# Kernel optimization log

Measured on AMD Instinct MI355X. Metric: run time of the kernel, lower is better.

Reference implementation:

```python
import jax, jax.numpy as jnp
import numpy as np

B, N, T, D, E, M = 8, 512, 64, 128, 32, 3


def _norm(v):
    return v / jnp.clip(jnp.linalg.norm(v, axis=-1, keepdims=True), 1e-12)


def setup_inputs() -> dict:
    key = jax.random.key(0)
    ks = jax.random.split(key, 14)
    s = 0.05
    x = jax.random.normal(ks[0], (B, N, T, 1), jnp.float32)
    # set_prior: binarized adjacency + self loops, row-normalized
    a = (jax.random.uniform(ks[1], (N, N)) > 0.95).astype(jnp.float32) + jnp.eye(N, dtype=jnp.float32)
    prior = a / jnp.clip(a.sum(1, keepdims=True), 1e-8)
    # orthogonal queries, as in torch __init__ (QR of zero-padded randn)
    rng = np.random.default_rng(0)
    qs = []
    for _ in range(M):
        pad = np.zeros((D, D), np.float32)
        pad[:E] = rng.standard_normal((E, D)).astype(np.float32) * 0.1
        q, _ = np.linalg.qr(pad)
        qs.append(q[:E])
    return {
        "x": x,
        "prior": prior,
        "proj_W": jax.random.normal(ks[2], (D, 1), jnp.float32) * s,
        "proj_b": jnp.zeros((D,), jnp.float32),
        "W_ih": jax.random.normal(ks[3], (3 * D, D), jnp.float32) * s,
        "W_hh": jax.random.normal(ks[4], (3 * D, D), jnp.float32) * s,
        "b_ih": jnp.zeros((3 * D,), jnp.float32),
        "b_hh": jnp.zeros((3 * D,), jnp.float32),
        "space_W": jax.random.normal(ks[5], (M, D, D), jnp.float32) * s,
        "space_b": jnp.zeros((M, D), jnp.float32),
        "router_W": jax.random.normal(ks[6], (M, 2 * D), jnp.float32) * s,
        "router_b": jnp.zeros((M,), jnp.float32),
        "out_W": jax.random.normal(ks[7], (1, D), jnp.float32) * s,
        "out_b": jnp.zeros((1,), jnp.float32),
        "prior_logit": jnp.array(1.0, jnp.float32),
        "queries": jnp.asarray(np.stack(qs)),  # [M, E, D]
    }


def reference(x, prior, proj_W, proj_b, W_ih, W_hh, b_ih, b_hh,
              space_W, space_b, router_W, router_b, out_W, out_b,
              prior_logit, queries):
    b, n, t, _ = x.shape
    d = proj_b.shape[0]
    m, e, _ = queries.shape
    # proj(x.permute(0,2,1,3)).reshape(B*N, T, D)  (faithful reshape of [B,T,N,D])
    hp = jnp.transpose(x, (0, 2, 1, 3)) @ proj_W.T + proj_b  # [B,T,N,D]
    seq = hp.reshape(b * n, t, d)
    xs = jnp.swapaxes(seq, 0, 1)  # [T, BN, D]

    def gru_step(h, xt):
        gi = xt @ W_ih.T + b_ih
        gh = h @ W_hh.T + b_hh
        ir, iz, i_n = jnp.split(gi, 3, axis=-1)
        hr, hz, h_n = jnp.split(gh, 3, axis=-1)
        r = jax.nn.sigmoid(ir + hr)
        z = jax.nn.sigmoid(iz + hz)
        ng = jnp.tanh(i_n + r * h_n)
        return (1.0 - z) * ng + z * h, None

    h, _ = jax.lax.scan(gru_step, jnp.zeros((b * n, d), x.dtype), xs)
    h = h.reshape(b, n, d)

    stats = jnp.concatenate([h.mean(1), jnp.std(h, axis=1, ddof=1)], axis=-1)  # torch std is unbiased
    probs = jax.nn.softmax(stats @ router_W.T + router_b, axis=-1)  # [B,M]

    z_prior = jnp.einsum('ij,bjd->bid', prior, h)

    hs = _norm(jnp.einsum('bnd,mkd->bmnk', h, space_W) + space_b[None, :, None, :])  # [B,M,N,D]
    q = _norm(queries)  # [M,E,D]
    scores = jnp.einsum('bmnd,med->bmen', hs, q)  # [B,M,E,N] (topk over N axis)
    k = min(n, max(4, int(n * 0.05)))
    vals, idx = jax.lax.top_k(scores, k)  # [B,M,E,k]
    w = jax.nn.softmax(vals / 0.7, axis=-1)
    H = jnp.zeros((b, m, e, n), h.dtype).at[
        jnp.arange(b)[:, None, None, None],
        jnp.arange(m)[None, :, None, None],
        jnp.arange(e)[None, None, :, None],
        idx,
    ].set(w)  # [B,M,E,N], transposed layout of torch's [B,N,E]

    Hmix = jnp.einsum('bmen,bm->ben', H, probs)  # [B,E,N] == torch Hmix^T
    edge = jnp.einsum('ben,bnd->bed', Hmix, h)   # Hmix^T @ h
    z_learn = jnp.einsum('ben,bed->bnd', Hmix, edge)  # Hmix @ edge

    alpha = jax.nn.sigmoid(prior_logit)
    out = (alpha * z_prior + (1.0 - alpha) * z_learn) @ out_W.T + out_b  # [B,N,1]
    return out.squeeze(-1), probs
```

## Files before the change

kernel.cpp:

```cpp
#include <hip/hip_runtime.h>
#include <math.h>

#define OFF_U      0
#define OFF_C      384
#define OFF_QWHI   768
#define OFF_QWLO   6912
#define OFF_H      13056
#define OFF_PROBS  537344
#define OFF_HV     537376
#define OFF_SCORES 541472
#define OFF_HMIX   934688
#define OFF_WHI    1066016
#define OFF_SHI    1115168
#define OFF_SLO    1139744
#define OFF_STATS  1164320
#define OFF_EV     1229856
#define OFF_QB     1230112

#define L2E_F 1.44269504088896340736f

typedef short bf16x8 __attribute__((ext_vector_type(8)));
typedef float f32x4 __attribute__((ext_vector_type(4)));

union U8 { unsigned short s[8]; bf16x8 v; uint4 u4; };

__device__ __forceinline__ unsigned short bf16_rtn(float f) {
  unsigned int u = __float_as_uint(f);
  return (unsigned short)((u + 0x7FFFu + ((u >> 16) & 1u)) >> 16);
}
__device__ __forceinline__ float bf16_f(unsigned short h) {
  return __uint_as_float(((unsigned int)h) << 16);
}

__global__ __launch_bounds__(256) void prep_kernel(const float* __restrict__ Wih,
                                                   const float* __restrict__ projW,
                                                   const float* __restrict__ projb,
                                                   const float* __restrict__ bih,
                                                   const float* __restrict__ queries,
                                                   const float* __restrict__ Whh,
                                                   const float* __restrict__ spaceW,
                                                   const float* __restrict__ spaceb,
                                                   float* __restrict__ ws) {
  const int bid = blockIdx.x, tid = threadIdx.x;
  const int wave = tid >> 6, lane = tid & 63;
  if (bid < 96) {
    int r = bid * 4 + wave;
    float w0 = Wih[r * 128 + lane], w1 = Wih[r * 128 + 64 + lane];
    float u = w0 * projW[lane] + w1 * projW[64 + lane];
    float c = w0 * projb[lane] + w1 * projb[64 + lane];
    for (int off = 32; off; off >>= 1) {
      u += __shfl_xor(u, off);
      c += __shfl_xor(c, off);
    }
    if (lane == 0) {
      ws[OFF_U + r] = u;
      ws[OFF_C + r] = c + bih[r];
    }
  } else if (bid < 112) {
    unsigned short* WHI = (unsigned short*)(ws + OFF_WHI);
    int base = (bid - 96) * 3072;
    for (int i = tid; i < 3072; i += 256) {
      int idx = base + i;
      float sc = (idx < 32768) ? L2E_F : (2.f * L2E_F);
      WHI[idx] = bf16_rtn(Whh[idx] * sc);
    }
  } else if (bid < 128) {
    unsigned short* SHI = (unsigned short*)(ws + OFF_SHI);
    unsigned short* SLO = (unsigned short*)(ws + OFF_SLO);
    int base = (bid - 112) * 3072;
    for (int i = tid; i < 3072; i += 256) {
      float w = spaceW[base + i];
      unsigned short hi = bf16_rtn(w);
      SHI[base + i] = hi;
      SLO[base + i] = bf16_rtn(w - bf16_f(hi));
    }
  } else if (bid < 224) {
    int qi = bid - 128;
    int m = qi >> 5, e = qi & 31;
    __shared__ float invS, qdS;
    const float* qrow = queries + (m * 32 + e) * 128;
    if (wave == 0) {
      float v0 = qrow[lane], v1 = qrow[64 + lane];
      float ss = v0 * v0 + v1 * v1;
      for (int off = 32; off; off >>= 1) ss += __shfl_xor(ss, off);
      if (lane == 0) invS = 1.f / fmaxf(sqrtf(ss), 1e-12f);
    } else if (wave == 1) {
      float v = qrow[lane] * spaceb[m * 128 + lane] +
                qrow[64 + lane] * spaceb[m * 128 + 64 + lane];
      for (int off = 32; off; off >>= 1) v += __shfl_xor(v, off);
      if (lane == 0) qdS = v;
    }
    __syncthreads();
    if (tid < 128) {
      int din = tid;
      float acc = 0.f;
      for (int dout = 0; dout < 128; ++dout)
        acc += qrow[dout] * spaceW[m * 16384 + dout * 128 + din];
      acc *= invS;
      unsigned short hi = bf16_rtn(acc);
      ((unsigned short*)(ws + OFF_QWHI))[(m * 32 + e) * 128 + din] = hi;
      ((unsigned short*)(ws + OFF_QWLO))[(m * 32 + e) * 128 + din] =
          bf16_rtn(acc - bf16_f(hi));
    }
    if (tid == 255) ws[OFF_QB + m * 32 + e] = qdS * invS;
  } else {
    ws[OFF_EV + tid] = 0.f;
    for (int i = tid; i < 2048; i += 256) ws[OFF_STATS + i] = 0.f;
  }
}

#define GRU_STEP(RB, WB, XSV)                                                       \
  do {                                                                              \
    f32x4 acc0 = c0i, acc1 = c1i, acc2 = c2i;                                       \
    _Pragma("unroll") for (int c = 0; c < 4; ++c) {                                 \
      bf16x8 Bf = *(const bf16x8*)&hB[RB][rdOff + c * 32];                          \
      acc0 = __builtin_amdgcn_mfma_f32_16x16x32_bf16(Bf, Ah[0][c], acc0, 0, 0, 0);  \
      acc1 = __builtin_amdgcn_mfma_f32_16x16x32_bf16(Bf, Ah[1][c], acc1, 0, 0, 0);  \
      acc2 = __builtin_amdgcn_mfma_f32_16x16x32_bf16(Bf, Ah[2][c], acc2, 0, 0, 0);  \
    }                                                                               \
    const float xsv = (XSV);                                                        \
    float hv[4];                                                                    \
    _Pragma("unroll") for (int r = 0; r < 4; ++r) {                                 \
      float gr = fmaf(xsv, ur[r], acc0[r]);                                         \
      float gz = fmaf(xsv, uz[r], acc1[r]);                                         \
      float gn = fmaf(xsv, un[r], cnv[r]);                                          \
      float rr = __builtin_amdgcn_rcpf(1.f + __builtin_amdgcn_exp2f(-gr));          \
      float Ez = __builtin_amdgcn_exp2f(gz);                                        \
      float a = fmaf(rr, acc2[r], gn);                                              \
      float Ea = __builtin_amdgcn_exp2f(a);                                         \
      float u = Ea + 1.f;                                                           \
      float v = Ez + 1.f;                                                           \
      float num = fmaf(1.f - hreg[r], u, -2.f);                                     \
      float hvv = fmaf(num, __builtin_amdgcn_rcpf(u * v), hreg[r]);                 \
      hv[r] = hvv;                                                                  \
      hreg[r] = hvv;                                                                \
    }                                                                               \
    unsigned int pk0, pk1;                                                          \
    asm("v_cvt_pk_bf16_f32 %0, %1, %2" : "=v"(pk0) : "v"(hv[0]), "v"(hv[1]));       \
    asm("v_cvt_pk_bf16_f32 %0, %1, %2" : "=v"(pk1) : "v"(hv[2]), "v"(hv[3]));       \
    *(uint2*)&hB[WB][wrOff] = make_uint2(pk0, pk1);                                 \
    __syncthreads();                                                                \
  } while (0)

__global__ __launch_bounds__(512, 2) void gru_kernel(const float* __restrict__ x,
                                                     const float* __restrict__ bhh,
                                                     const float* __restrict__ outW,
                                                     float* __restrict__ ws) {
  __shared__ __align__(16) unsigned short hB[2][16 * 136];
  __shared__ __align__(16) float xsAll[16 * 68];
  __shared__ float hFin[16 * 132];

  const int tid = threadIdx.x, wave = tid >> 6, lane = tid & 63;
  const int q = lane >> 4, s15 = lane & 15;
  const int d0 = wave * 16 + q * 4;
  const unsigned short* WHI = (const unsigned short*)(ws + OFF_WHI);

  {
    float4 z4 = make_float4(0.f, 0.f, 0.f, 0.f);
    float4* hm4 = (float4*)(ws + OFF_HMIX);
    if (tid < 128) hm4[blockIdx.x * 128 + tid] = z4;
  }

  bf16x8 Ah[3][4];
#pragma unroll
  for (int t = 0; t < 3; ++t) {
    int row = (wave + 8 * t) * 16 + s15;
#pragma unroll
    for (int c = 0; c < 4; ++c)
      Ah[t][c] = *(const bf16x8*)&WHI[row * 128 + c * 32 + q * 8];
  }

  float ur[4], uz[4], un[4], cnv[4];
  f32x4 c0i, c1i, c2i;
#pragma unroll
  for (int r = 0; r < 4; ++r) {
    int d = d0 + r;
    ur[r] = ws[OFF_U + d] * L2E_F;
    uz[r] = ws[OFF_U + 128 + d] * L2E_F;
    un[r] = ws[OFF_U + 256 + d] * (2.f * L2E_F);
    c0i[r] = (ws[OFF_C + d] + bhh[d]) * L2E_F;
    c1i[r] = (ws[OFF_C + 128 + d] + bhh[128 + d]) * L2E_F;
    cnv[r] = ws[OFF_C + 256 + d] * (2.f * L2E_F);
    c2i[r] = bhh[256 + d] * (2.f * L2E_F);
  }

  const int seq0 = blockIdx.x * 16;
  for (int i = tid; i < 1024; i += 512) {
    int s = i >> 6, tt = i & 63;
    int r = (seq0 + s) * 64 + tt;
    xsAll[s * 68 + tt] = x[((r >> 15) * 512 + (r & 511)) * 64 + ((r >> 9) & 63)];
  }
  for (int i = tid; i < 2176; i += 512) hB[0][i] = 0;
  __syncthreads();

  float hreg[4] = {0.f, 0.f, 0.f, 0.f};
  const int rdOff = s15 * 136 + q * 8;
  const int wrOff = s15 * 136 + d0;
  const int xsOff = s15 * 68;

#pragma unroll 1
  for (int t4 = 0; t4 < 16; ++t4) {
    const float4 xs4 = *(const float4*)&xsAll[xsOff + t4 * 4];
    GRU_STEP(0, 1, xs4.x);
    GRU_STEP(1, 0, xs4.y);
    GRU_STEP(0, 1, xs4.z);
    GRU_STEP(1, 0, xs4.w);
  }

#pragma unroll
  for (int r = 0; r < 4; ++r) hFin[s15 * 132 + d0 + r] = hreg[r];
  __syncthreads();
  float* h_out = ws + OFF_H;
#pragma unroll
  for (int p = 0; p < 4; ++p) {
    int item = tid + p * 512;
    int s = item >> 7, dd = item & 127;
    h_out[(seq0 + s) * 128 + dd] = hFin[s * 132 + dd];
  }
  for (int s = wave * 2; s < wave * 2 + 2; ++s) {
    float a = hFin[s * 132 + lane] * outW[lane] + hFin[s * 132 + 64 + lane] * outW[64 + lane];
    for (int off = 32; off; off >>= 1) a += __shfl_xor(a, off);
    if (lane == 0) ws[OFF_HV + seq0 + s] = a;
  }
  if (tid < 128) {
    float s = 0.f, q2 = 0.f;
#pragma unroll
    for (int sI = 0; sI < 16; ++sI) {
      float v = hFin[sI * 132 + tid];
      s += v; q2 += v * v;
    }
    int b = blockIdx.x >> 5;
    atomicAdd(&ws[OFF_STATS + b * 256 + tid], s);
    atomicAdd(&ws[OFF_STATS + b * 256 + 128 + tid], q2);
  }
}

__global__ __launch_bounds__(256) void scores_kernel(const float* __restrict__ spaceb,
                                                     const float* __restrict__ routerW,
                                                     const float* __restrict__ routerb,
                                                     float* __restrict__ ws,
                                                     float* __restrict__ d_out) {
  const int bid = blockIdx.x;
  const int chunk = bid & 15, m = (bid >> 4) % 3, b = bid / 48;
  const int n0 = chunk * 32;
  const int tid = threadIdx.x, wave = tid >> 6, lane = tid & 63;
  const int q = lane >> 4, s15 = lane & 15;

  __shared__ __align__(16) unsigned short sHi[16 * 33 * 8];
  __shared__ __align__(16) unsigned short sLo[16 * 33 * 8];
  __shared__ float hsL[32 * 132];
  __shared__ float biasL[128];
  __shared__ float invnL[32];
  __shared__ float qbL[32];

  const float* hG = ws + OFF_H;
  const unsigned short* SHI = (const unsigned short*)(ws + OFF_SHI);
  const unsigned short* SLO = (const unsigned short*)(ws + OFF_SLO);
  const unsigned short* QWHI = (const unsigned short*)(ws + OFF_QWHI);
  const unsigned short* QWLO = (const unsigned short*)(ws + OFF_QWLO);

  if (tid < 128) biasL[tid] = spaceb[m * 128 + tid];
  else if (tid < 160) qbL[tid - 128] = ws[OFF_QB + m * 32 + (tid - 128)];
  {
    int nn = tid >> 3, kc = tid & 7;
    const float* row = &hG[(b * 512 + n0 + nn) * 128 + kc * 16];
    U8 ph0, pl0, ph1, pl1;
#pragma unroll
    for (int j = 0; j < 8; ++j) {
      float v = row[j];
      unsigned short hi = bf16_rtn(v);
      ph0.s[j] = hi; pl0.s[j] = bf16_rtn(v - bf16_f(hi));
    }
#pragma unroll
    for (int j = 0; j < 8; ++j) {
      float v = row[8 + j];
      unsigned short hi = bf16_rtn(v);
      ph1.s[j] = hi; pl1.s[j] = bf16_rtn(v - bf16_f(hi));
    }
    int g0 = kc * 2;
    *(uint4*)&sHi[(g0 * 33 + nn) * 8] = ph0.u4;
    *(uint4*)&sLo[(g0 * 33 + nn) * 8] = pl0.u4;
    *(uint4*)&sHi[((g0 + 1) * 33 + nn) * 8] = ph1.u4;
    *(uint4*)&sLo[((g0 + 1) * 33 + nn) * 8] = pl1.u4;
  }
  __syncthreads();

  const int nt = wave >> 1;
  const int half = wave & 1;
  const int dt0 = half * 4;
  f32x4 acc[4] = {{0.f,0.f,0.f,0.f},{0.f,0.f,0.f,0.f},{0.f,0.f,0.f,0.f},{0.f,0.f,0.f,0.f}};
  f32x4 accS = {0.f, 0.f, 0.f, 0.f};
#pragma unroll
  for (int c = 0; c < 4; ++c) {
    bf16x8 Ahi = *(const bf16x8*)&sHi[((c * 4 + q) * 33 + nt * 16 + s15) * 8];
    bf16x8 Alo = *(const bf16x8*)&sLo[((c * 4 + q) * 33 + nt * 16 + s15) * 8];
#pragma unroll
    for (int i = 0; i < 4; ++i) {
      int row = m * 16384 + ((dt0 + i) * 16 + s15) * 128 + c * 32 + q * 8;
      bf16x8 Bhi = *(const bf16x8*)&SHI[row];
      bf16x8 Blo = *(const bf16x8*)&SLO[row];
      acc[i] = __builtin_amdgcn_mfma_f32_16x16x32_bf16(Ahi, Bhi, acc[i], 0, 0, 0);
      acc[i] = __builtin_amdgcn_mfma_f32_16x16x32_bf16(Alo, Bhi, acc[i], 0, 0, 0);
      acc[i] = __builtin_amdgcn_mfma_f32_16x16x32_bf16(Ahi, Blo, acc[i], 0, 0, 0);
    }
    {
      int row = (m * 32 + half * 16 + s15) * 128 + c * 32 + q * 8;
      bf16x8 Qhi = *(const bf16x8*)&QWHI[row];
      bf16x8 Qlo = *(const bf16x8*)&QWLO[row];
      accS = __builtin_amdgcn_mfma_f32_16x16x32_bf16(Ahi, Qhi, accS, 0, 0, 0);
      accS = __builtin_amdgcn_mfma_f32_16x16x32_bf16(Alo, Qhi, accS, 0, 0, 0);
      accS = __builtin_amdgcn_mfma_f32_16x16x32_bf16(Ahi, Qlo, accS, 0, 0, 0);
    }
  }
#pragma unroll
  for (int i = 0; i < 4; ++i) {
    int dcol = (dt0 + i) * 16 + s15;
    float bb = biasL[dcol];
#pragma unroll
    for (int r = 0; r < 4; ++r)
      hsL[(nt * 16 + q * 4 + r) * 132 + dcol] = acc[i][r] + bb;
  }
  __syncthreads();

  {
    int n = tid >> 3, kc = tid & 7;
    float ss = 0.f;
#pragma unroll
    for (int d4 = 0; d4 < 4; ++d4) {
      float4 v = *(const float4*)&hsL[n * 132 + kc * 16 + d4 * 4];
      ss += v.x * v.x + v.y * v.y + v.z * v.z + v.w * v.w;
    }
    ss += __shfl_xor(ss, 1); ss += __shfl_xor(ss, 2); ss += __shfl_xor(ss, 4);
    if (kc == 0) invnL[n] = 1.f / fmaxf(sqrtf(ss), 1e-12f);
  }
  __syncthreads();

  {
    int e = half * 16 + s15;
    float qb = qbL[e];
    int nb = nt * 16 + q * 4;
    float4 o;
    o.x = (accS[0] + qb) * invnL[nb + 0];
    o.y = (accS[1] + qb) * invnL[nb + 1];
    o.z = (accS[2] + qb) * invnL[nb + 2];
    o.w = (accS[3] + qb) * invnL[nb + 3];
    *(float4*)&ws[OFF_SCORES + ((b * 3 + m) * 32 + e) * 512 + n0 + nb] = o;
  }

  if ((bid % 48) == 0) {
    __syncthreads();
    float* st = hsL;
    float* lgS = hsL + 256;
    if (tid < 128) {
      float s = ws[OFF_STATS + b * 256 + tid];
      float q2 = ws[OFF_STATS + b * 256 + 128 + tid];
      float mean = s * (1.f / 512.f);
      float var = (q2 - 512.f * mean * mean) * (1.f / 511.f);
      st[tid] = mean;
      st[128 + tid] = sqrtf(fmaxf(var, 0.f));
    }
    __syncthreads();
    if (tid < 192) {
      int w = tid >> 6, ln = tid & 63;
      float acc2 = 0.f;
#pragma unroll
      for (int j = 0; j < 4; ++j)
        acc2 += st[ln * 4 + j] * routerW[w * 256 + ln * 4 + j];
      for (int off = 32; off; off >>= 1) acc2 += __shfl_xor(acc2, off);
      if (ln == 0) lgS[w] = acc2 + routerb[w];
    }
    __syncthreads();
    if (tid == 0) {
      float mx = fmaxf(lgS[0], fmaxf(lgS[1], lgS[2]));
      float e0 = expf(lgS[0] - mx), e1 = expf(lgS[1] - mx), e2 = expf(lgS[2] - mx);
      float inv = 1.f / (e0 + e1 + e2);
      ws[OFF_PROBS + b * 3 + 0] = e0 * inv;
      ws[OFF_PROBS + b * 3 + 1] = e1 * inv;
      ws[OFF_PROBS + b * 3 + 2] = e2 * inv;
      d_out[4096 + b * 3 + 0] = e0 * inv;
      d_out[4096 + b * 3 + 1] = e1 * inv;
      d_out[4096 + b * 3 + 2] = e2 * inv;
    }
  }
}

__global__ __launch_bounds__(256) void topk_kernel(float* __restrict__ ws) {
  const int row0 = blockIdx.x * 4;
  const int b = row0 / 96;
  const int tid = threadIdx.x, wave = tid >> 6, lane = tid & 63;
  __shared__ float hvL[512];
  hvL[tid] = ws[OFF_HV + b * 512 + tid];
  hvL[256 + tid] = ws[OFF_HV + b * 512 + 256 + tid];
  __syncthreads();

  int row = row0 + wave;
  int m = (row / 32) % 3, e = row & 31;
  const float* sc = ws + OFF_SCORES + row * 512;
  float prob = ws[OFF_PROBS + b * 3 + m];

  float v[8];
#pragma unroll
  for (int j = 0; j < 8; ++j) v[j] = sc[j * 64 + lane];

  float selv = 0.f; int seli = 0; float maxv = 0.f;
  for (int it = 0; it < 25; ++it) {
    float bv = v[0]; int bj = 0;
#pragma unroll
    for (int j = 1; j < 8; ++j)
      if (v[j] > bv) { bv = v[j]; bj = j; }
    int bidx = bj * 64 + lane;
    for (int off = 32; off; off >>= 1) {
      float ov = __shfl_xor(bv, off);
      int oi = __shfl_xor(bidx, off);
      if (ov > bv || (ov == bv && oi < bidx)) { bv = ov; bidx = oi; }
    }
    if (lane == (bidx & 63)) v[bidx >> 6] = -INFINITY;
    if (it == 0) maxv = bv;
    if (lane == it) { selv = bv; seli = bidx; }
  }
  float ex = (lane < 25) ? __expf((selv - maxv) * (1.f / 0.7f)) : 0.f;
  float den = ex;
  for (int off = 32; off; off >>= 1) den += __shfl_xor(den, off);
  float w = prob * ex / den;
  if (lane < 25)
    atomicAdd(&ws[OFF_HMIX + (b * 32 + e) * 512 + seli], w);
  float evc = (lane < 25) ? w * hvL[seli] : 0.f;
  for (int off = 32; off; off >>= 1) evc += __shfl_xor(evc, off);
  if (lane == 0) atomicAdd(&ws[OFF_EV + b * 32 + e], evc);
}

__global__ __launch_bounds__(512) void final_kernel(const float* __restrict__ prior,
                                                    const float* __restrict__ outb,
                                                    const float* __restrict__ plog,
                                                    float* __restrict__ ws,
                                                    float* __restrict__ d_out) {
  const int bid = blockIdx.x;
  const int b = bid >> 4, ch = bid & 15;
  const int tid = threadIdx.x, wave = tid >> 6, lane = tid & 63;
  __shared__ float hvL[512], evL[32];
  hvL[tid] = ws[OFF_HV + b * 512 + tid];
  if (tid < 32) evL[tid] = ws[OFF_EV + b * 32 + tid];
  __syncthreads();
  float alpha = 1.f / (1.f + expf(-plog[0]));
  float ob = outb[0];
#pragma unroll
  for (int i = 0; i < 4; ++i) {
    int n = ch * 32 + wave * 4 + i;
    const float* pr = prior + n * 512;
    float s1 = 0.f;
#pragma unroll
    for (int j = 0; j < 8; ++j) s1 += pr[j * 64 + lane] * hvL[j * 64 + lane];
    float s2 = 0.f;
    if (lane < 32) s2 = ws[OFF_HMIX + (b * 32 + lane) * 512 + n] * evL[lane];
    float a = alpha * s1 + (1.f - alpha) * s2;
    for (int off = 32; off; off >>= 1) a += __shfl_xor(a, off);
    if (lane == 0) d_out[b * 512 + n] = a + ob;
  }
}

extern "C" void kernel_launch(void* const* d_in, const int* in_sizes, int n_in,
                              void* d_out, int out_size, void* d_ws, size_t ws_size,
                              hipStream_t stream) {
  const float* x       = (const float*)d_in[0];
  const float* prior   = (const float*)d_in[1];
  const float* projW   = (const float*)d_in[2];
  const float* projb   = (const float*)d_in[3];
  const float* Wih     = (const float*)d_in[4];
  const float* Whh     = (const float*)d_in[5];
  const float* bih     = (const float*)d_in[6];
  const float* bhh     = (const float*)d_in[7];
  const float* spaceW  = (const float*)d_in[8];
  const float* spaceb  = (const float*)d_in[9];
  const float* routerW = (const float*)d_in[10];
  const float* routerb = (const float*)d_in[11];
  const float* outW    = (const float*)d_in[12];
  const float* outb    = (const float*)d_in[13];
  const float* plog    = (const float*)d_in[14];
  const float* queries = (const float*)d_in[15];
  float* ws  = (float*)d_ws;
  float* out = (float*)d_out;

  prep_kernel<<<225, 256, 0, stream>>>(Wih, projW, projb, bih, queries, Whh,
                                       spaceW, spaceb, ws);
  gru_kernel<<<256, 512, 0, stream>>>(x, bhh, outW, ws);
  scores_kernel<<<384, 256, 0, stream>>>(spaceb, routerW, routerb, ws, out);
  topk_kernel<<<192, 256, 0, stream>>>(ws);
  final_kernel<<<128, 512, 0, stream>>>(prior, outb, plog, ws, out);
}
```

Measured before the change: 162.2 us.

## Fuse scores, topk and final kernels into one persistent kernel with grid barriers

Merges the scores, top-k and final kernels into a single launch of 384 blocks, separated by global atomic-counter barriers with spin-waits. Blocks that finish early exit at each phase (192 run top-k, 128 run the final stage, each now covering 8 rows per wave). The aim is to drop two kernel launch gaps. In exchange it relies on all 384 blocks being co-resident to avoid deadlock, and the spin-waits add polling cost.

```diff
diff --git a/kernel.cpp b/kernel.cpp
--- a/kernel.cpp
+++ b/kernel.cpp
@@ -16,6 +16,7 @@
 #define OFF_STATS  1164320
 #define OFF_EV     1229856
 #define OFF_QB     1230112
+#define OFF_SYNC   1230208
 
 #define L2E_F 1.44269504088896340736f
 
@@ -106,6 +107,7 @@
   } else {
     ws[OFF_EV + tid] = 0.f;
     for (int i = tid; i < 2048; i += 256) ws[OFF_STATS + i] = 0.f;
+    if (tid < 2) ((unsigned int*)(ws + OFF_SYNC))[tid] = 0u;
   }
 }
 
@@ -235,14 +237,15 @@
   }
 }
 
-__global__ __launch_bounds__(256) void scores_kernel(const float* __restrict__ spaceb,
-                                                     const float* __restrict__ routerW,
-                                                     const float* __restrict__ routerb,
-                                                     float* __restrict__ ws,
-                                                     float* __restrict__ d_out) {
+__global__ __launch_bounds__(256) void fused_kernel(const float* __restrict__ spaceb,
+                                                    const float* __restrict__ routerW,
+                                                    const float* __restrict__ routerb,
+                                                    const float* __restrict__ prior,
+                                                    const float* __restrict__ outb,
+                                                    const float* __restrict__ plog,
+                                                    float* __restrict__ ws,
+                                                    float* __restrict__ d_out) {
   const int bid = blockIdx.x;
-  const int chunk = bid & 15, m = (bid >> 4) % 3, b = bid / 48;
-  const int n0 = chunk * 32;
   const int tid = threadIdx.x, wave = tid >> 6, lane = tid & 63;
   const int q = lane >> 4, s15 = lane & 15;
 
@@ -252,209 +255,237 @@
   __shared__ float biasL[128];
   __shared__ float invnL[32];
   __shared__ float qbL[32];
-
-  const float* hG = ws + OFF_H;
-  const unsigned short* SHI = (const unsigned short*)(ws + OFF_SHI);
-  const unsigned short* SLO = (const unsigned short*)(ws + OFF_SLO);
-  const unsigned short* QWHI = (const unsigned short*)(ws + OFF_QWHI);
-  const unsigned short* QWLO = (const unsigned short*)(ws + OFF_QWLO);
-
-  if (tid < 128) biasL[tid] = spaceb[m * 128 + tid];
-  else if (tid < 160) qbL[tid - 128] = ws[OFF_QB + m * 32 + (tid - 128)];
+  __shared__ float hvT[512];
+  __shared__ float hvF[512];
+  __shared__ float evL[32];
+
+  unsigned int* cnt = (unsigned int*)(ws + OFF_SYNC);
+
   {
-    int nn = tid >> 3, kc = tid & 7;
-    const float* row = &hG[(b * 512 + n0 + nn) * 128 + kc * 16];
-    U8 ph0, pl0, ph1, pl1;
-#pragma unroll
-    for (int j = 0; j < 8; ++j) {
-      float v = row[j];
-      unsigned short hi = bf16_rtn(v);
-      ph0.s[j] = hi; pl0.s[j] = bf16_rtn(v - bf16_f(hi));
-    }
-#pragma unroll
-    for (int j = 0; j < 8; ++j) {
-      float v = row[8 + j];
-      unsigned short hi = bf16_rtn(v);
-      ph1.s[j] = hi; pl1.s[j] = bf16_rtn(v - bf16_f(hi));
-    }
-    int g0 = kc * 2;
-    *(uint4*)&sHi[(g0 * 33 + nn) * 8] = ph0.u4;
-    *(uint4*)&sLo[(g0 * 33 + nn) * 8] = pl0.u4;
-    *(uint4*)&sHi[((g0 + 1) * 33 + nn) * 8] = ph1.u4;
-    *(uint4*)&sLo[((g0 + 1) * 33 + nn) * 8] = pl1.u4;
-  }
+    const int chunk = bid & 15, m = (bid >> 4) % 3, b = bid / 48;
+    const int n0 = chunk * 32;
+
+    const float* hG = ws + OFF_H;
+    const unsigned short* SHI = (const unsigned short*)(ws + OFF_SHI);
+    const unsigned short* SLO = (const unsigned short*)(ws + OFF_SLO);
+    const unsigned short* QWHI = (const unsigned short*)(ws + OFF_QWHI);
+    const unsigned short* QWLO = (const unsigned short*)(ws + OFF_QWLO);
+
+    if (tid < 128) biasL[tid] = spaceb[m * 128 + tid];
+    else if (tid < 160) qbL[tid - 128] = ws[OFF_QB + m * 32 + (tid - 128)];
+    {
+      int nn = tid >> 3, kc = tid & 7;
+      const float* row = &hG[(b * 512 + n0 + nn) * 128 + kc * 16];
+      U8 ph0, pl0, ph1, pl1;
+#pragma unroll
+      for (int j = 0; j < 8; ++j) {
+        float v = row[j];
+        unsigned short hi = bf16_rtn(v);
+        ph0.s[j] = hi; pl0.s[j] = bf16_rtn(v - bf16_f(hi));
+      }
+#pragma unroll
+      for (int j = 0; j < 8; ++j) {
+        float v = row[8 + j];
+        unsigned short hi = bf16_rtn(v);
+        ph1.s[j] = hi; pl1.s[j] = bf16_rtn(v - bf16_f(hi));
+      }
+      int g0 = kc * 2;
+      *(uint4*)&sHi[(g0 * 33 + nn) * 8] = ph0.u4;
+      *(uint4*)&sLo[(g0 * 33 + nn) * 8] = pl0.u4;
+      *(uint4*)&sHi[((g0 + 1) * 33 + nn) * 8] = ph1.u4;
+      *(uint4*)&sLo[((g0 + 1) * 33 + nn) * 8] = pl1.u4;
+    }
+    __syncthreads();
+
+    const int nt = wave >> 1;
+    const int half = wave & 1;
+    const int dt0 = half * 4;
+    f32x4 acc[4] = {{0.f,0.f,0.f,0.f},{0.f,0.f,0.f,0.f},{0.f,0.f,0.f,0.f},{0.f,0.f,0.f,0.f}};
+    f32x4 accS = {0.f, 0.f, 0.f, 0.f};
+#pragma unroll
+    for (int c = 0; c < 4; ++c) {
+      bf16x8 Ahi = *(const bf16x8*)&sHi[((c * 4 + q) * 33 + nt * 16 + s15) * 8];
+      bf16x8 Alo = *(const bf16x8*)&sLo[((c * 4 + q) * 33 + nt * 16 + s15) * 8];
+#pragma unroll
+      for (int i = 0; i < 4; ++i) {
+        int row = m * 16384 + ((dt0 + i) * 16 + s15) * 128 + c * 32 + q * 8;
+        bf16x8 Bhi = *(const bf16x8*)&SHI[row];
+        bf16x8 Blo = *(const bf16x8*)&SLO[row];
+        acc[i] = __builtin_amdgcn_mfma_f32_16x16x32_bf16(Ahi, Bhi, acc[i], 0, 0, 0);
+        acc[i] = __builtin_amdgcn_mfma_f32_16x16x32_bf16(Alo, Bhi, acc[i], 0, 0, 0);
+        acc[i] = __builtin_amdgcn_mfma_f32_16x16x32_bf16(Ahi, Blo, acc[i], 0, 0, 0);
+      }
+      {
+        int row = (m * 32 + half * 16 + s15) * 128 + c * 32 + q * 8;
+        bf16x8 Qhi = *(const bf16x8*)&QWHI[row];
+        bf16x8 Qlo = *(const bf16x8*)&QWLO[row];
+        accS = __builtin_amdgcn_mfma_f32_16x16x32_bf16(Ahi, Qhi, accS, 0, 0, 0);
+        accS = __builtin_amdgcn_mfma_f32_16x16x32_bf16(Alo, Qhi, accS, 0, 0, 0);
+        accS = __builtin_amdgcn_mfma_f32_16x16x32_bf16(Ahi, Qlo, accS, 0, 0, 0);
+      }
+    }
+#pragma unroll
+    for (int i = 0; i < 4; ++i) {
+      int dcol = (dt0 + i) * 16 + s15;
+      float bb = biasL[dcol];
+#pragma unroll
+      for (int r = 0; r < 4; ++r)
+        hsL[(nt * 16 + q * 4 + r) * 132 + dcol] = acc[i][r] + bb;
+    }
+    __syncthreads();
+
+    {
+      int n = tid >> 3, kc = tid & 7;
+      float ss = 0.f;
+#pragma unroll
+      for (int d4 = 0; d4 < 4; ++d4) {
+        float4 v = *(const float4*)&hsL[n * 132 + kc * 16 + d4 * 4];
+        ss += v.x * v.x + v.y * v.y + v.z * v.z + v.w * v.w;
+      }
+      ss += __shfl_xor(ss, 1); ss += __shfl_xor(ss, 2); ss += __shfl_xor(ss, 4);
+      if (kc == 0) invnL[n] = 1.f / fmaxf(sqrtf(ss), 1e-12f);
+    }
+    __syncthreads();
+
+    {
+      int e = half * 16 + s15;
+      float qb = qbL[e];
+      int nb = nt * 16 + q * 4;
+      float4 o;
+      o.x = (accS[0] + qb) * invnL[nb + 0];
+      o.y = (accS[1] + qb) * invnL[nb + 1];
+      o.z = (accS[2] + qb) * invnL[nb + 2];
+      o.w = (accS[3] + qb) * invnL[nb + 3];
+      *(float4*)&ws[OFF_SCORES + ((b * 3 + m) * 32 + e) * 512 + n0 + nb] = o;
+    }
+
+    if ((bid % 48) == 0) {
+      __syncthreads();
+      float* st = hsL;
+      float* lgS = hsL + 256;
+      if (tid < 128) {
+        float s = ws[OFF_STATS + b * 256 + tid];
+        float q2 = ws[OFF_STATS + b * 256 + 128 + tid];
+        float mean = s * (1.f / 512.f);
+        float var = (q2 - 512.f * mean * mean) * (1.f / 511.f);
+        st[tid] = mean;
+        st[128 + tid] = sqrtf(fmaxf(var, 0.f));
+      }
+      __syncthreads();
+      if (tid < 192) {
+        int w = tid >> 6, ln = tid & 63;
+        float acc2 = 0.f;
+#pragma unroll
+        for (int j = 0; j < 4; ++j)
+          acc2 += st[ln * 4 + j] * routerW[w * 256 + ln * 4 + j];
+        for (int off = 32; off; off >>= 1) acc2 += __shfl_xor(acc2, off);
+        if (ln == 0) lgS[w] = acc2 + routerb[w];
+      }
+      __syncthreads();
+      if (tid == 0) {
+        float mx = fmaxf(lgS[0], fmaxf(lgS[1], lgS[2]));
+        float e0 = expf(lgS[0] - mx), e1 = expf(lgS[1] - mx), e2 = expf(lgS[2] - mx);
+        float inv = 1.f / (e0 + e1 + e2);
+        ws[OFF_PROBS + b * 3 + 0] = e0 * inv;
+        ws[OFF_PROBS + b * 3 + 1] = e1 * inv;
+        ws[OFF_PROBS + b * 3 + 2] = e2 * inv;
+        d_out[4096 + b * 3 + 0] = e0 * inv;
+        d_out[4096 + b * 3 + 1] = e1 * inv;
+        d_out[4096 + b * 3 + 2] = e2 * inv;
+      }
+    }
+  }
+
   __syncthreads();
-
-  const int nt = wave >> 1;
-  const int half = wave & 1;
-  const int dt0 = half * 4;
-  f32x4 acc[4] = {{0.f,0.f,0.f,0.f},{0.f,0.f,0.f,0.f},{0.f,0.f,0.f,0.f},{0.f,0.f,0.f,0.f}};
-  f32x4 accS = {0.f, 0.f, 0.f, 0.f};
-#pragma unroll
-  for (int c = 0; c < 4; ++c) {
-    bf16x8 Ahi = *(const bf16x8*)&sHi[((c * 4 + q) * 33 + nt * 16 + s15) * 8];
-    bf16x8 Alo = *(const bf16x8*)&sLo[((c * 4 + q) * 33 + nt * 16 + s15) * 8];
-#pragma unroll
-    for (int i = 0; i < 4; ++i) {
-      int row = m * 16384 + ((dt0 + i) * 16 + s15) * 128 + c * 32 + q * 8;
-      bf16x8 Bhi = *(const bf16x8*)&SHI[row];
-      bf16x8 Blo = *(const bf16x8*)&SLO[row];
-      acc[i] = __builtin_amdgcn_mfma_f32_16x16x32_bf16(Ahi, Bhi, acc[i], 0, 0, 0);
-      acc[i] = __builtin_amdgcn_mfma_f32_16x16x32_bf16(Alo, Bhi, acc[i], 0, 0, 0);
-      acc[i] = __builtin_amdgcn_mfma_f32_16x16x32_bf16(Ahi, Blo, acc[i], 0, 0, 0);
-    }
-    {
-      int row = (m * 32 + half * 16 + s15) * 128 + c * 32 + q * 8;
-      bf16x8 Qhi = *(const bf16x8*)&QWHI[row];
-      bf16x8 Qlo = *(const bf16x8*)&QWLO[row];
-      accS = __builtin_amdgcn_mfma_f32_16x16x32_bf16(Ahi, Qhi, accS, 0, 0, 0);
-      accS = __builtin_amdgcn_mfma_f32_16x16x32_bf16(Alo, Qhi, accS, 0, 0, 0);
-      accS = __builtin_amdgcn_mfma_f32_16x16x32_bf16(Ahi, Qlo, accS, 0, 0, 0);
-    }
-  }
-#pragma unroll
-  for (int i = 0; i < 4; ++i) {
-    int dcol = (dt0 + i) * 16 + s15;
-    float bb = biasL[dcol];
-#pragma unroll
-    for (int r = 0; r < 4; ++r)
-      hsL[(nt * 16 + q * 4 + r) * 132 + dcol] = acc[i][r] + bb;
+  if (tid == 0) {
+    __threadfence();
+    atomicAdd(&cnt[0], 1u);
+  }
+  if (bid >= 192) return;
+  if (tid == 0) {
+    while (__hip_atomic_load(&cnt[0], __ATOMIC_RELAXED, __HIP_MEMORY_SCOPE_AGENT) < 384u)
+      __builtin_amdgcn_s_sleep(10);
+    __threadfence();
   }
   __syncthreads();
 
   {
-    int n = tid >> 3, kc = tid & 7;
-    float ss = 0.f;
-#pragma unroll
-    for (int d4 = 0; d4 < 4; ++d4) {
-      float4 v = *(const float4*)&hsL[n * 132 + kc * 16 + d4 * 4];
-      ss += v.x * v.x + v.y * v.y + v.z * v.z + v.w * v.w;
-    }
-    ss += __shfl_xor(ss, 1); ss += __shfl_xor(ss, 2); ss += __shfl_xor(ss, 4);
-    if (kc == 0) invnL[n] = 1.f / fmaxf(sqrtf(ss), 1e-12f);
-  }
+    const int row0 = bid * 4;
+    const int b = row0 / 96;
+    hvT[tid] = ws[OFF_HV + b * 512 + tid];
+    hvT[256 + tid] = ws[OFF_HV + b * 512 + 256 + tid];
+    __syncthreads();
+
+    int row = row0 + wave;
+    int m = (row / 32) % 3, e = row & 31;
+    const float* sc = ws + OFF_SCORES + row * 512;
+    float prob = ws[OFF_PROBS + b * 3 + m];
+
+    float v[8];
+#pragma unroll
+    for (int j = 0; j < 8; ++j) v[j] = sc[j * 64 + lane];
+
+    float selv = 0.f; int seli = 0; float maxv = 0.f;
+    for (int it = 0; it < 25; ++it) {
+      float bv = v[0]; int bj = 0;
+#pragma unroll
+      for (int j = 1; j < 8; ++j)
+        if (v[j] > bv) { bv = v[j]; bj = j; }
+      int bidx = bj * 64 + lane;
+      for (int off = 32; off; off >>= 1) {
+        float ov = __shfl_xor(bv, off);
+        int oi = __shfl_xor(bidx, off);
+        if (ov > bv || (ov == bv && oi < bidx)) { bv = ov; bidx = oi; }
+      }
+      if (lane == (bidx & 63)) v[bidx >> 6] = -INFINITY;
+      if (it == 0) maxv = bv;
+      if (lane == it) { selv = bv; seli = bidx; }
+    }
+    float ex = (lane < 25) ? __expf((selv - maxv) * (1.f / 0.7f)) : 0.f;
+    float den = ex;
+    for (int off = 32; off; off >>= 1) den += __shfl_xor(den, off);
+    float w = prob * ex / den;
+    if (lane < 25)
+      atomicAdd(&ws[OFF_HMIX + (b * 32 + e) * 512 + seli], w);
+    float evc = (lane < 25) ? w * hvT[seli] : 0.f;
+    for (int off = 32; off; off >>= 1) evc += __shfl_xor(evc, off);
+    if (lane == 0) atomicAdd(&ws[OFF_EV + b * 32 + e], evc);
+  }
+
   __syncthreads();
+  if (tid == 0) {
+    __threadfence();
+    atomicAdd(&cnt[1], 1u);
+  }
+  if (bid >= 128) return;
+  if (tid == 0) {
+    while (__hip_atomic_load(&cnt[1], __ATOMIC_RELAXED, __HIP_MEMORY_SCOPE_AGENT) < 192u)
+      __builtin_amdgcn_s_sleep(10);
+    __threadfence();
+  }
+  __syncthreads();
 
   {
-    int e = half * 16 + s15;
-    float qb = qbL[e];
-    int nb = nt * 16 + q * 4;
-    float4 o;
-    o.x = (accS[0] + qb) * invnL[nb + 0];
-    o.y = (accS[1] + qb) * invnL[nb + 1];
-    o.z = (accS[2] + qb) * invnL[nb + 2];
-    o.w = (accS[3] + qb) * invnL[nb + 3];
-    *(float4*)&ws[OFF_SCORES + ((b * 3 + m) * 32 + e) * 512 + n0 + nb] = o;
-  }
-
-  if ((bid % 48) == 0) {
+    const int b = bid >> 4, ch = bid & 15;
+    hvF[tid] = ws[OFF_HV + b * 512 + tid];
+    hvF[256 + tid] = ws[OFF_HV + b * 512 + 256 + tid];
+    if (tid < 32) evL[tid] = ws[OFF_EV + b * 32 + tid];
     __syncthreads();
-    float* st = hsL;
-    float* lgS = hsL + 256;
-    if (tid < 128) {
-      float s = ws[OFF_STATS + b * 256 + tid];
-      float q2 = ws[OFF_STATS + b * 256 + 128 + tid];
-      float mean = s * (1.f / 512.f);
-      float var = (q2 - 512.f * mean * mean) * (1.f / 511.f);
-      st[tid] = mean;
-      st[128 + tid] = sqrtf(fmaxf(var, 0.f));
-    }
-    __syncthreads();
-    if (tid < 192) {
-      int w = tid >> 6, ln = tid & 63;
-      float acc2 = 0.f;
-#pragma unroll
-      for (int j = 0; j < 4; ++j)
-        acc2 += st[ln * 4 + j] * routerW[w * 256 + ln * 4 + j];
-      for (int off = 32; off; off >>= 1) acc2 += __shfl_xor(acc2, off);
-      if (ln == 0) lgS[w] = acc2 + routerb[w];
-    }
-    __syncthreads();
-    if (tid == 0) {
-      float mx = fmaxf(lgS[0], fmaxf(lgS[1], lgS[2]));
-      float e0 = expf(lgS[0] - mx), e1 = expf(lgS[1] - mx), e2 = expf(lgS[2] - mx);
-      float inv = 1.f / (e0 + e1 + e2);
-      ws[OFF_PROBS + b * 3 + 0] = e0 * inv;
-      ws[OFF_PROBS + b * 3 + 1] = e1 * inv;
-      ws[OFF_PROBS + b * 3 + 2] = e2 * inv;
-      d_out[4096 + b * 3 + 0] = e0 * inv;
-      d_out[4096 + b * 3 + 1] = e1 * inv;
-      d_out[4096 + b * 3 + 2] = e2 * inv;
-    }
-  }
-}
-
-__global__ __launch_bounds__(256) void topk_kernel(float* __restrict__ ws) {
-  const int row0 = blockIdx.x * 4;
-  const int b = row0 / 96;
-  const int tid = threadIdx.x, wave = tid >> 6, lane = tid & 63;
-  __shared__ float hvL[512];
-  hvL[tid] = ws[OFF_HV + b * 512 + tid];
-  hvL[256 + tid] = ws[OFF_HV + b * 512 + 256 + tid];
-  __syncthreads();
-
-  int row = row0 + wave;
-  int m = (row / 32) % 3, e = row & 31;
-  const float* sc = ws + OFF_SCORES + row * 512;
-  float prob = ws[OFF_PROBS + b * 3 + m];
-
-  float v[8];
-#pragma unroll
-  for (int j = 0; j < 8; ++j) v[j] = sc[j * 64 + lane];
-
-  float selv = 0.f; int seli = 0; float maxv = 0.f;
-  for (int it = 0; it < 25; ++it) {
-    float bv = v[0]; int bj = 0;
-#pragma unroll
-    for (int j = 1; j < 8; ++j)
-      if (v[j] > bv) { bv = v[j]; bj = j; }
-    int bidx = bj * 64 + lane;
-    for (int off = 32; off; off >>= 1) {
-      float ov = __shfl_xor(bv, off);
-      int oi = __shfl_xor(bidx, off);
-      if (ov > bv || (ov == bv && oi < bidx)) { bv = ov; bidx = oi; }
-    }
-    if (lane == (bidx & 63)) v[bidx >> 6] = -INFINITY;
-    if (it == 0) maxv = bv;
-    if (lane == it) { selv = bv; seli = bidx; }
-  }
-  float ex = (lane < 25) ? __expf((selv - maxv) * (1.f / 0.7f)) : 0.f;
-  float den = ex;
-  for (int off = 32; off; off >>= 1) den += __shfl_xor(den, off);
-  float w = prob * ex / den;
-  if (lane < 25)
-    atomicAdd(&ws[OFF_HMIX + (b * 32 + e) * 512 + seli], w);
-  float evc = (lane < 25) ? w * hvL[seli] : 0.f;
-  for (int off = 32; off; off >>= 1) evc += __shfl_xor(evc, off);
-  if (lane == 0) atomicAdd(&ws[OFF_EV + b * 32 + e], evc);
-}
-
-__global__ __launch_bounds__(512) void final_kernel(const float* __restrict__ prior,
-                                                    const float* __restrict__ outb,
-                                                    const float* __restrict__ plog,
-                                                    float* __restrict__ ws,
-                                                    float* __restrict__ d_out) {
-  const int bid = blockIdx.x;
-  const int b = bid >> 4, ch = bid & 15;
-  const int tid = threadIdx.x, wave = tid >> 6, lane = tid & 63;
-  __shared__ float hvL[512], evL[32];
-  hvL[tid] = ws[OFF_HV + b * 512 + tid];
-  if (tid < 32) evL[tid] = ws[OFF_EV + b * 32 + tid];
-  __syncthreads();
-  float alpha = 1.f / (1.f + expf(-plog[0]));
-  float ob = outb[0];
-#pragma unroll
-  for (int i = 0; i < 4; ++i) {
-    int n = ch * 32 + wave * 4 + i;
-    const float* pr = prior + n * 512;
-    float s1 = 0.f;
-#pragma unroll
-    for (int j = 0; j < 8; ++j) s1 += pr[j * 64 + lane] * hvL[j * 64 + lane];
-    float s2 = 0.f;
-    if (lane < 32) s2 = ws[OFF_HMIX + (b * 32 + lane) * 512 + n] * evL[lane];
-    float a = alpha * s1 + (1.f - alpha) * s2;
-    for (int off = 32; off; off >>= 1) a += __shfl_xor(a, off);
-    if (lane == 0) d_out[b * 512 + n] = a + ob;
+    float alpha = 1.f / (1.f + expf(-plog[0]));
+    float ob = outb[0];
+#pragma unroll
+    for (int i = 0; i < 8; ++i) {
+      int n = ch * 32 + wave * 8 + i;
+      const float* pr = prior + n * 512;
+      float s1 = 0.f;
+#pragma unroll
+      for (int j = 0; j < 8; ++j) s1 += pr[j * 64 + lane] * hvF[j * 64 + lane];
+      float s2 = 0.f;
+      if (lane < 32) s2 = ws[OFF_HMIX + (b * 32 + lane) * 512 + n] * evL[lane];
+      float a = alpha * s1 + (1.f - alpha) * s2;
+      for (int off = 32; off; off >>= 1) a += __shfl_xor(a, off);
+      if (lane == 0) d_out[b * 512 + n] = a + ob;
+    }
   }
 }
 
@@ -483,7 +514,6 @@
   prep_kernel<<<225, 256, 0, stream>>>(Wih, projW, projb, bih, queries, Whh,
                                        spaceW, spaceb, ws);
   gru_kernel<<<256, 512, 0, stream>>>(x, bhh, outW, ws);
-  scores_kernel<<<384, 256, 0, stream>>>(spaceb, routerW, routerb, ws, out);
-  topk_kernel<<<192, 256, 0, stream>>>(ws);
-  final_kernel<<<128, 512, 0, stream>>>(prior, outb, plog, ws, out);
+  fused_kernel<<<384, 256, 0, stream>>>(spaceb, routerW, routerb, prior, outb,
+                                        plog, ws, out);
 }
```

Measured after the change: 196.1 us. 1.21x slower.

## Fold prep kernel into GRU kernel and replace stats atomics with per-block partials

Applied to the files above, without the earlier changes.

Removes the separate prep launch. Each GRU block now computes the input-projection vectors and converts its W_hh fragments to bf16 directly into registers. 24 extra blocks appended to the GRU grid handle the space-weight split and the query-weight products. The per-batch stats atomics are replaced by per-block partial writes that the scores kernel sums. This saves a launch and the workspace round-trip, at the cost of redundant per-block Wih reductions (48 rows per wave) in every GRU block.

```diff
diff --git a/kernel.cpp b/kernel.cpp
--- a/kernel.cpp
+++ b/kernel.cpp
@@ -1,8 +1,6 @@
 #include <hip/hip_runtime.h>
 #include <math.h>
 
-#define OFF_U      0
-#define OFF_C      384
 #define OFF_QWHI   768
 #define OFF_QWLO   6912
 #define OFF_H      13056
@@ -10,7 +8,6 @@
 #define OFF_HV     537376
 #define OFF_SCORES 541472
 #define OFF_HMIX   934688
-#define OFF_WHI    1066016
 #define OFF_SHI    1115168
 #define OFF_SLO    1139744
 #define OFF_STATS  1164320
@@ -30,83 +27,6 @@
 }
 __device__ __forceinline__ float bf16_f(unsigned short h) {
   return __uint_as_float(((unsigned int)h) << 16);
-}
-
-__global__ __launch_bounds__(256) void prep_kernel(const float* __restrict__ Wih,
-                                                   const float* __restrict__ projW,
-                                                   const float* __restrict__ projb,
-                                                   const float* __restrict__ bih,
-                                                   const float* __restrict__ queries,
-                                                   const float* __restrict__ Whh,
-                                                   const float* __restrict__ spaceW,
-                                                   const float* __restrict__ spaceb,
-                                                   float* __restrict__ ws) {
-  const int bid = blockIdx.x, tid = threadIdx.x;
-  const int wave = tid >> 6, lane = tid & 63;
-  if (bid < 96) {
-    int r = bid * 4 + wave;
-    float w0 = Wih[r * 128 + lane], w1 = Wih[r * 128 + 64 + lane];
-    float u = w0 * projW[lane] + w1 * projW[64 + lane];
-    float c = w0 * projb[lane] + w1 * projb[64 + lane];
-    for (int off = 32; off; off >>= 1) {
-      u += __shfl_xor(u, off);
-      c += __shfl_xor(c, off);
-    }
-    if (lane == 0) {
-      ws[OFF_U + r] = u;
-      ws[OFF_C + r] = c + bih[r];
-    }
-  } else if (bid < 112) {
-    unsigned short* WHI = (unsigned short*)(ws + OFF_WHI);
-    int base = (bid - 96) * 3072;
-    for (int i = tid; i < 3072; i += 256) {
-      int idx = base + i;
-      float sc = (idx < 32768) ? L2E_F : (2.f * L2E_F);
-      WHI[idx] = bf16_rtn(Whh[idx] * sc);
-    }
-  } else if (bid < 128) {
-    unsigned short* SHI = (unsigned short*)(ws + OFF_SHI);
-    unsigned short* SLO = (unsigned short*)(ws + OFF_SLO);
-    int base = (bid - 112) * 3072;
-    for (int i = tid; i < 3072; i += 256) {
-      float w = spaceW[base + i];
-      unsigned short hi = bf16_rtn(w);
-      SHI[base + i] = hi;
-      SLO[base + i] = bf16_rtn(w - bf16_f(hi));
-    }
-  } else if (bid < 224) {
-    int qi = bid - 128;
-    int m = qi >> 5, e = qi & 31;
-    __shared__ float invS, qdS;
-    const float* qrow = queries + (m * 32 + e) * 128;
-    if (wave == 0) {
-      float v0 = qrow[lane], v1 = qrow[64 + lane];
-      float ss = v0 * v0 + v1 * v1;
-      for (int off = 32; off; off >>= 1) ss += __shfl_xor(ss, off);
-      if (lane == 0) invS = 1.f / fmaxf(sqrtf(ss), 1e-12f);
-    } else if (wave == 1) {
-      float v = qrow[lane] * spaceb[m * 128 + lane] +
-                qrow[64 + lane] * spaceb[m * 128 + 64 + lane];
-      for (int off = 32; off; off >>= 1) v += __shfl_xor(v, off);
-      if (lane == 0) qdS = v;
-    }
-    __syncthreads();
-    if (tid < 128) {
-      int din = tid;
-      float acc = 0.f;
-      for (int dout = 0; dout < 128; ++dout)
-        acc += qrow[dout] * spaceW[m * 16384 + dout * 128 + din];
-      acc *= invS;
-      unsigned short hi = bf16_rtn(acc);
-      ((unsigned short*)(ws + OFF_QWHI))[(m * 32 + e) * 128 + din] = hi;
-      ((unsigned short*)(ws + OFF_QWLO))[(m * 32 + e) * 128 + din] =
-          bf16_rtn(acc - bf16_f(hi));
-    }
-    if (tid == 255) ws[OFF_QB + m * 32 + e] = qdS * invS;
-  } else {
-    ws[OFF_EV + tid] = 0.f;
-    for (int i = tid; i < 2048; i += 256) ws[OFF_STATS + i] = 0.f;
-  }
 }
 
 #define GRU_STEP(RB, WB, XSV)                                                       \
@@ -145,43 +65,118 @@
 __global__ __launch_bounds__(512, 2) void gru_kernel(const float* __restrict__ x,
                                                      const float* __restrict__ bhh,
                                                      const float* __restrict__ outW,
+                                                     const float* __restrict__ Wih,
+                                                     const float* __restrict__ projW,
+                                                     const float* __restrict__ projb,
+                                                     const float* __restrict__ bih,
+                                                     const float* __restrict__ Whh,
+                                                     const float* __restrict__ queries,
+                                                     const float* __restrict__ spaceW,
+                                                     const float* __restrict__ spaceb,
                                                      float* __restrict__ ws) {
   __shared__ __align__(16) unsigned short hB[2][16 * 136];
   __shared__ __align__(16) float xsAll[16 * 68];
   __shared__ float hFin[16 * 132];
+  __shared__ float qrowL[4][128];
+  __shared__ float invS4[4], qdS4[4];
 
   const int tid = threadIdx.x, wave = tid >> 6, lane = tid & 63;
+
+  if (blockIdx.x >= 256) {
+    const int bid2 = blockIdx.x - 256;
+    {
+      unsigned short* SHI = (unsigned short*)(ws + OFF_SHI);
+      unsigned short* SLO = (unsigned short*)(ws + OFF_SLO);
+      int base = bid2 * 2048;
+#pragma unroll
+      for (int p = 0; p < 4; ++p) {
+        int i = base + tid + p * 512;
+        float w = spaceW[i];
+        unsigned short hi = bf16_rtn(w);
+        SHI[i] = hi;
+        SLO[i] = bf16_rtn(w - bf16_f(hi));
+      }
+    }
+    if (bid2 == 0 && tid < 256) ws[OFF_EV + tid] = 0.f;
+    const int g = tid >> 7, dtid = tid & 127;
+    const int qi = bid2 * 4 + g, m = qi >> 5;
+    qrowL[g][dtid] = queries[qi * 128 + dtid];
+    __syncthreads();
+    {
+      int gg = wave >> 1;
+      int qig = bid2 * 4 + gg, mg = qig >> 5;
+      float v0 = qrowL[gg][lane], v1 = qrowL[gg][64 + lane];
+      if ((wave & 1) == 0) {
+        float ss = v0 * v0 + v1 * v1;
+        for (int off = 32; off; off >>= 1) ss += __shfl_xor(ss, off);
+        if (lane == 0) invS4[gg] = 1.f / fmaxf(sqrtf(ss), 1e-12f);
+      } else {
+        float v = v0 * spaceb[mg * 128 + lane] + v1 * spaceb[mg * 128 + 64 + lane];
+        for (int off = 32; off; off >>= 1) v += __shfl_xor(v, off);
+        if (lane == 0) qdS4[gg] = v;
+      }
+    }
+    __syncthreads();
+    {
+      float acc = 0.f;
+      const float* sw = spaceW + m * 16384 + dtid;
+#pragma unroll 8
+      for (int dout = 0; dout < 128; ++dout)
+        acc = fmaf(qrowL[g][dout], sw[dout * 128], acc);
+      float a = acc * invS4[g];
+      unsigned short hi = bf16_rtn(a);
+      ((unsigned short*)(ws + OFF_QWHI))[qi * 128 + dtid] = hi;
+      ((unsigned short*)(ws + OFF_QWLO))[qi * 128 + dtid] = bf16_rtn(a - bf16_f(hi));
+      if (dtid == 0) ws[OFF_QB + qi] = qdS4[g] * invS4[g];
+    }
+    return;
+  }
+
   const int q = lane >> 4, s15 = lane & 15;
   const int d0 = wave * 16 + q * 4;
-  const unsigned short* WHI = (const unsigned short*)(ws + OFF_WHI);
+
+  {
+    float pw0 = projW[lane], pw1 = projW[64 + lane];
+    float pb0 = projb[lane], pb1 = projb[64 + lane];
+    for (int i = 0; i < 48; ++i) {
+      int row = wave * 48 + i;
+      float w0 = Wih[row * 128 + lane], w1 = Wih[row * 128 + 64 + lane];
+      float uu = w0 * pw0 + w1 * pw1;
+      float cc = w0 * pb0 + w1 * pb1;
+      for (int off = 32; off; off >>= 1) {
+        uu += __shfl_xor(uu, off);
+        cc += __shfl_xor(cc, off);
+      }
+      if (lane == 0) {
+        hFin[row] = uu;
+        hFin[512 + row] = cc;
+      }
+    }
+  }
+
+  bf16x8 Ah[3][4];
+#pragma unroll
+  for (int t = 0; t < 3; ++t) {
+    const float sc = (t == 2) ? (2.f * L2E_F) : L2E_F;
+    int row = (wave + 8 * t) * 16 + s15;
+#pragma unroll
+    for (int c = 0; c < 4; ++c) {
+      const float* src = &Whh[row * 128 + c * 32 + q * 8];
+      float4 f0 = *(const float4*)src;
+      float4 f1 = *(const float4*)(src + 4);
+      U8 pk;
+      pk.s[0] = bf16_rtn(f0.x * sc); pk.s[1] = bf16_rtn(f0.y * sc);
+      pk.s[2] = bf16_rtn(f0.z * sc); pk.s[3] = bf16_rtn(f0.w * sc);
+      pk.s[4] = bf16_rtn(f1.x * sc); pk.s[5] = bf16_rtn(f1.y * sc);
+      pk.s[6] = bf16_rtn(f1.z * sc); pk.s[7] = bf16_rtn(f1.w * sc);
+      Ah[t][c] = pk.v;
+    }
+  }
 
   {
     float4 z4 = make_float4(0.f, 0.f, 0.f, 0.f);
     float4* hm4 = (float4*)(ws + OFF_HMIX);
     if (tid < 128) hm4[blockIdx.x * 128 + tid] = z4;
-  }
-
-  bf16x8 Ah[3][4];
-#pragma unroll
-  for (int t = 0; t < 3; ++t) {
-    int row = (wave + 8 * t) * 16 + s15;
-#pragma unroll
-    for (int c = 0; c < 4; ++c)
-      Ah[t][c] = *(const bf16x8*)&WHI[row * 128 + c * 32 + q * 8];
-  }
-
-  float ur[4], uz[4], un[4], cnv[4];
-  f32x4 c0i, c1i, c2i;
-#pragma unroll
-  for (int r = 0; r < 4; ++r) {
-    int d = d0 + r;
-    ur[r] = ws[OFF_U + d] * L2E_F;
-    uz[r] = ws[OFF_U + 128 + d] * L2E_F;
-    un[r] = ws[OFF_U + 256 + d] * (2.f * L2E_F);
-    c0i[r] = (ws[OFF_C + d] + bhh[d]) * L2E_F;
-    c1i[r] = (ws[OFF_C + 128 + d] + bhh[128 + d]) * L2E_F;
-    cnv[r] = ws[OFF_C + 256 + d] * (2.f * L2E_F);
-    c2i[r] = bhh[256 + d] * (2.f * L2E_F);
   }
 
   const int seq0 = blockIdx.x * 16;
@@ -191,6 +186,31 @@
     xsAll[s * 68 + tt] = x[((r >> 15) * 512 + (r & 511)) * 64 + ((r >> 9) & 63)];
   }
   for (int i = tid; i < 2176; i += 512) hB[0][i] = 0;
+  __syncthreads();
+
+  float ur[4], uz[4], un[4], cnv[4];
+  f32x4 c0i, c1i, c2i;
+  {
+    float4 bi0 = *(const float4*)&bih[d0];
+    float4 bi1 = *(const float4*)&bih[128 + d0];
+    float4 bi2 = *(const float4*)&bih[256 + d0];
+    float4 bh0 = *(const float4*)&bhh[d0];
+    float4 bh1 = *(const float4*)&bhh[128 + d0];
+    float4 bh2 = *(const float4*)&bhh[256 + d0];
+    const float* biP[3] = {(const float*)&bi0, (const float*)&bi1, (const float*)&bi2};
+    const float* bhP[3] = {(const float*)&bh0, (const float*)&bh1, (const float*)&bh2};
+#pragma unroll
+    for (int r = 0; r < 4; ++r) {
+      int d = d0 + r;
+      ur[r] = hFin[d] * L2E_F;
+      uz[r] = hFin[128 + d] * L2E_F;
+      un[r] = hFin[256 + d] * (2.f * L2E_F);
+      c0i[r] = (hFin[512 + d] + biP[0][r] + bhP[0][r]) * L2E_F;
+      c1i[r] = (hFin[512 + 128 + d] + biP[1][r] + bhP[1][r]) * L2E_F;
+      cnv[r] = (hFin[512 + 256 + d] + biP[2][r]) * (2.f * L2E_F);
+      c2i[r] = bhP[2][r] * (2.f * L2E_F);
+    }
+  }
   __syncthreads();
 
   float hreg[4] = {0.f, 0.f, 0.f, 0.f};
@@ -229,9 +249,8 @@
       float v = hFin[sI * 132 + tid];
       s += v; q2 += v * v;
     }
-    int b = blockIdx.x >> 5;
-    atomicAdd(&ws[OFF_STATS + b * 256 + tid], s);
-    atomicAdd(&ws[OFF_STATS + b * 256 + 128 + tid], q2);
+    ws[OFF_STATS + blockIdx.x * 256 + tid] = s;
+    ws[OFF_STATS + blockIdx.x * 256 + 128 + tid] = q2;
   }
 }
 
@@ -352,8 +371,12 @@
     float* st = hsL;
     float* lgS = hsL + 256;
     if (tid < 128) {
-      float s = ws[OFF_STATS + b * 256 + tid];
-      float q2 = ws[OFF_STATS + b * 256 + 128 + tid];
+      float s = 0.f, q2 = 0.f;
+      const float* base = ws + OFF_STATS + b * 32 * 256;
+      for (int j = 0; j < 32; ++j) {
+        s += base[j * 256 + tid];
+        q2 += base[j * 256 + 128 + tid];
+      }
       float mean = s * (1.f / 512.f);
       float var = (q2 - 512.f * mean * mean) * (1.f / 511.f);
       st[tid] = mean;
@@ -480,9 +503,8 @@
   float* ws  = (float*)d_ws;
   float* out = (float*)d_out;
 
-  prep_kernel<<<225, 256, 0, stream>>>(Wih, projW, projb, bih, queries, Whh,
-                                       spaceW, spaceb, ws);
-  gru_kernel<<<256, 512, 0, stream>>>(x, bhh, outW, ws);
+  gru_kernel<<<280, 512, 0, stream>>>(x, bhh, outW, Wih, projW, projb, bih,
+                                      Whh, queries, spaceW, spaceb, ws);
   scores_kernel<<<384, 256, 0, stream>>>(spaceb, routerW, routerb, ws, out);
   topk_kernel<<<192, 256, 0, stream>>>(ws);
   final_kernel<<<128, 512, 0, stream>>>(prior, outb, plog, ws, out);
```

Measured after the change: 188.7 us. +16.4%, slower.
